# Performance work log

Measured on AMD Instinct MI355X. Metric: run time of the kernel, lower is better.

Reference implementation:

```python
import jax, jax.numpy as jnp
import numpy as np

DIM = 1024
HEADS = 16
HEAD_DIM = DIM // HEADS
SCALE = DIM ** (-0.5)  # note: module scales by full dim, not head_dim


def setup_inputs() -> dict:
    key = jax.random.key(0)
    k1, k2, k3, k4 = jax.random.split(key, 4)
    B, N = 4, 2048
    x = jax.random.normal(k1, (B, N, DIM), dtype=jnp.float32)
    # nn.Linear(dim, 3*dim, bias=False): weight [3*dim, dim]
    w_qkv = jax.random.normal(k2, (3 * DIM, DIM), dtype=jnp.float32) * (DIM ** -0.5)
    # nn.Linear(dim, dim) with bias
    w_out = jax.random.normal(k3, (DIM, DIM), dtype=jnp.float32) * (DIM ** -0.5)
    b_out = jax.random.normal(k4, (DIM,), dtype=jnp.float32) * 0.01
    return {"x": x, "w_qkv": w_qkv, "w_out": w_out, "b_out": b_out}


def reference(x, w_qkv, w_out, b_out):
    b, n, _ = x.shape
    qkv = jnp.einsum('bnd,ed->bne', x, w_qkv)  # [b, n, 3*dim]
    # rearrange 'b n (qkv h d) -> qkv b h n d'
    qkv = qkv.reshape(b, n, 3, HEADS, HEAD_DIM)
    q, k, v = (qkv[:, :, i].transpose(0, 2, 1, 3) for i in range(3))  # [b, h, n, d]
    dots = jnp.einsum('bhid,bhjd->bhij', q, k) * SCALE
    attn = jax.nn.softmax(dots, axis=-1)
    out = jnp.einsum('bhij,bhjd->bhid', attn, v)
    out = out.transpose(0, 2, 1, 3).reshape(b, n, HEADS * HEAD_DIM)  # [b, n, dim]
    return jnp.einsum('bnd,ed->bne', out, w_out) + b_out
```

## Files before the change

kernel.cpp:

```cpp
#include <hip/hip_runtime.h>

typedef __bf16 bf16_t;
typedef __bf16 bf16x2 __attribute__((ext_vector_type(2)));
typedef __bf16 bf16x4 __attribute__((ext_vector_type(4)));
typedef __bf16 bf16x8 __attribute__((ext_vector_type(8)));
typedef float floatx4 __attribute__((ext_vector_type(4)));

__device__ __forceinline__ void gll16(const void* g, void* l) {
  __builtin_amdgcn_global_load_lds(
      (const __attribute__((address_space(1))) void*)g,
      (__attribute__((address_space(3))) void*)l, 16, 0, 0);
}

__device__ __forceinline__ bf16x8 cvt8(const float4 a, const float4 b) {
  bf16x8 v;
  v[0] = (bf16_t)a.x; v[1] = (bf16_t)a.y; v[2] = (bf16_t)a.z; v[3] = (bf16_t)a.w;
  v[4] = (bf16_t)b.x; v[5] = (bf16_t)b.y; v[6] = (bf16_t)b.z; v[7] = (bf16_t)b.w;
  return v;
}

__global__ __launch_bounds__(256)
void cvt_f32_bf16(const float* __restrict__ src, bf16_t* __restrict__ dst, int n8)
{
  const int i = blockIdx.x * 256 + threadIdx.x;
  if (i < n8) {
    const float4 a = ((const float4*)src)[2 * i];
    const float4 b = ((const float4*)src)[2 * i + 1];
    *(bf16x8*)(dst + (size_t)i * 8) = cvt8(a, b);
  }
}

template<bool A32, bool W32, bool C32>
__global__ __launch_bounds__(256, 2)
void gemm_bt(const void* __restrict__ Av, const void* __restrict__ Wv,
             const float* __restrict__ bias, void* __restrict__ Cv,
             int M, int Nf, int K, int lda)
{
  __shared__ __align__(16) bf16_t lA[128 * 32];
  __shared__ __align__(16) bf16_t lB[128 * 32];

  const int tid  = threadIdx.x;
  const int wave = tid >> 6;
  const int lane = tid & 63;
  const int q    = lane >> 4;
  const int ln   = lane & 15;
  const int wm   = wave >> 1, wn = wave & 1;

  const int nwg = gridDim.x;
  const int bid = (blockIdx.x & 7) * (nwg >> 3) + (blockIdx.x >> 3);

  const int mtiles = M >> 7;
  const int mt = bid % mtiles;
  const int nt = bid / mtiles;
  const int m0 = mt << 7, n0 = nt << 7;

  floatx4 acc[4][4] = {};

  for (int k0 = 0; k0 < K; k0 += 32) {
    if constexpr (A32) {
      const float* Af = (const float*)Av;
#pragma unroll
      for (int sub = 0; sub < 2; ++sub) {
        const int r  = sub * 64 + (tid >> 2);
        const int c8 = tid & 3;
        const float* s = Af + (size_t)(m0 + r) * lda + k0 + c8 * 8;
        const float4 f0 = *(const float4*)s;
        const float4 f1 = *(const float4*)(s + 4);
        *(bf16x8*)(lA + r * 32 + (c8 ^ ((r >> 1) & 3)) * 8) = cvt8(f0, f1);
      }
    } else {
      const bf16_t* Ab = (const bf16_t*)Av;
#pragma unroll
      for (int half = 0; half < 2; ++half) {
        const int rbase = half * 64 + wave * 16;
        const int r  = rbase + (lane >> 2);
        const int gc = (lane & 3) ^ ((r >> 1) & 3);
        gll16(Ab + (size_t)(m0 + r) * lda + k0 + gc * 8, lA + rbase * 32);
      }
    }
    if constexpr (W32) {
      const float* Wf = (const float*)Wv;
#pragma unroll
      for (int sub = 0; sub < 2; ++sub) {
        const int r  = sub * 64 + (tid >> 2);
        const int c8 = tid & 3;
        const float* s = Wf + (size_t)(n0 + r) * K + k0 + c8 * 8;
        const float4 f0 = *(const float4*)s;
        const float4 f1 = *(const float4*)(s + 4);
        *(bf16x8*)(lB + r * 32 + (c8 ^ ((r >> 1) & 3)) * 8) = cvt8(f0, f1);
      }
    } else {
      const bf16_t* Wb = (const bf16_t*)Wv;
#pragma unroll
      for (int half = 0; half < 2; ++half) {
        const int rbase = half * 64 + wave * 16;
        const int r  = rbase + (lane >> 2);
        const int gc = (lane & 3) ^ ((r >> 1) & 3);
        gll16(Wb + (size_t)(n0 + r) * K + k0 + gc * 8, lB + rbase * 32);
      }
    }
    __syncthreads();

    bf16x8 af[4], bfr[4];
#pragma unroll
    for (int i = 0; i < 4; ++i) {
      const int r = wm * 64 + i * 16 + ln;
      af[i] = *(const bf16x8*)(lA + r * 32 + (q ^ ((r >> 1) & 3)) * 8);
    }
#pragma unroll
    for (int j = 0; j < 4; ++j) {
      const int r = wn * 64 + j * 16 + ln;
      bfr[j] = *(const bf16x8*)(lB + r * 32 + (q ^ ((r >> 1) & 3)) * 8);
    }
#pragma unroll
    for (int i = 0; i < 4; ++i)
#pragma unroll
      for (int j = 0; j < 4; ++j)
        acc[i][j] = __builtin_amdgcn_mfma_f32_16x16x32_bf16(af[i], bfr[j], acc[i][j], 0, 0, 0);
    __syncthreads();
  }

#pragma unroll
  for (int j = 0; j < 4; ++j) {
    const int col = n0 + wn * 64 + j * 16 + ln;
    const float bv = bias ? bias[col] : 0.0f;
#pragma unroll
    for (int i = 0; i < 4; ++i) {
      const int row = m0 + wm * 64 + i * 16 + q * 4;
#pragma unroll
      for (int r = 0; r < 4; ++r) {
        const float val = acc[i][j][r] + bv;
        if constexpr (C32)
          ((float*)Cv)[(size_t)(row + r) * Nf + col] = val;
        else
          ((bf16_t*)Cv)[(size_t)(row + r) * Nf + col] = (bf16_t)val;
      }
    }
  }
}

__global__ __launch_bounds__(256, 2)
void attn_kernel(bf16_t* __restrict__ qkv)
{
  __shared__ __align__(16) bf16_t lK[2][128 * 64];
  __shared__ __align__(16) bf16_t lVT[64 * 128];
  __shared__ __align__(16) bf16_t lP[128 * 128];

  const int tid  = threadIdx.x;
  const int wave = tid >> 6;
  const int lane = tid & 63;
  const int q  = lane >> 4;
  const int ln = lane & 15;
  const int wm = wave >> 1, wn = wave & 1;

  const int hw = blockIdx.x;
  const int w  = (hw & 7) * 128 + (hw >> 3);
  const int qt = w & 15;
  const int h  = (w >> 4) & 15;
  const int b  = w >> 8;

  bf16_t* Qbase = qkv + (size_t)(b * 2048 + qt * 128) * 3072 + h * 64;
  const bf16_t* Kbase = qkv + (size_t)(b * 2048) * 3072 + 1024 + h * 64;
  const bf16_t* Vbase = qkv + (size_t)(b * 2048) * 3072 + 2048 + h * 64;

#pragma unroll
  for (int t = 0; t < 4; ++t) {
    const int rbase = t * 32 + wave * 8;
    const int r  = rbase + (lane >> 3);
    const int gc = (lane & 7) ^ (r & 7);
    gll16(Qbase + (size_t)r * 3072 + gc * 8, lP + rbase * 64);
    gll16(Kbase + (size_t)r * 3072 + gc * 8, lK[0] + rbase * 64);
  }
  __syncthreads();

  bf16x8 qf[4][2];
#pragma unroll
  for (int i = 0; i < 4; ++i) {
    const int r = wm * 64 + i * 16 + ln;
#pragma unroll
    for (int kt = 0; kt < 2; ++kt) {
      const int c = (kt * 4 + q) ^ (r & 7);
      qf[i][kt] = *(const bf16x8*)(lP + r * 64 + c * 8);
    }
  }

  bf16x8 vcur[2][2], vnxt[2][2];
#pragma unroll
  for (int it = 0; it < 2; ++it) {
    const bf16_t* src = Vbase + (size_t)(2 * lane) * 3072 + (wave + it * 4) * 8;
    vcur[it][0] = *(const bf16x8*)src;
    vcur[it][1] = *(const bf16x8*)(src + 3072);
  }

  floatx4 accO[4][2] = {};
  floatx4 accS[4] = {};

  bf16x8 ones;
#pragma unroll
  for (int j = 0; j < 8; ++j) ones[j] = (bf16_t)1.0f;

  for (int jt = 0; jt < 16; ++jt) {
    const bf16_t* lKc = lK[jt & 1];
    bf16_t*       lKn = lK[(jt & 1) ^ 1];

    __syncthreads();

#pragma unroll
    for (int it = 0; it < 2; ++it) {
      const int c = wave + it * 4;
#pragma unroll
      for (int j = 0; j < 8; ++j) {
        const int d  = c * 8 + j;
        const int ch = (lane >> 2) ^ (d & 7);
        bf16x2 pr;
        pr[0] = vcur[it][0][j];
        pr[1] = vcur[it][1][j];
        *(bf16x2*)(lVT + d * 128 + ch * 8 + ((2 * lane) & 7)) = pr;
      }
    }

    bf16x8 kf[4][2];
#pragma unroll
    for (int n = 0; n < 4; ++n) {
      const int r = wn * 64 + n * 16 + ln;
#pragma unroll
      for (int kt = 0; kt < 2; ++kt) {
        const int c = (kt * 4 + q) ^ (r & 7);
        kf[n][kt] = *(const bf16x8*)(lKc + r * 64 + c * 8);
      }
    }

    if (jt < 15) {
      const int j0n = (jt + 1) * 128;
#pragma unroll
      for (int t = 0; t < 4; ++t) {
        const int rbase = t * 32 + wave * 8;
        const int r  = rbase + (lane >> 3);
        const int gc = (lane & 7) ^ (r & 7);
        gll16(Kbase + (size_t)(j0n + r) * 3072 + gc * 8, lKn + rbase * 64);
      }
#pragma unroll
      for (int it = 0; it < 2; ++it) {
        const bf16_t* src = Vbase + (size_t)(j0n + 2 * lane) * 3072 + (wave + it * 4) * 8;
        vnxt[it][0] = *(const bf16x8*)src;
        vnxt[it][1] = *(const bf16x8*)(src + 3072);
      }
    }

    __builtin_amdgcn_s_setprio(1);
#pragma unroll
    for (int i = 0; i < 4; ++i) {
#pragma unroll
      for (int n = 0; n < 4; ++n) {
        floatx4 st = {0.0f, 0.0f, 0.0f, 0.0f};
        st = __builtin_amdgcn_mfma_f32_16x16x32_bf16(kf[i][0], qf[n][0], st, 0, 0, 0);
        st = __builtin_amdgcn_mfma_f32_16x16x32_bf16(kf[i][1], qf[n][1], st, 0, 0, 0);
        bf16x4 pk;
#pragma unroll
        for (int r = 0; r < 4; ++r)
          pk[r] = (bf16_t)__builtin_amdgcn_exp2f(st[r] * 0.04508422f);
        const int m    = wm * 64 + n * 16 + ln;
        const int tok0 = wn * 64 + i * 16 + q * 4;
        *(bf16x4*)(lP + m * 128 + (((tok0 >> 3) ^ (m & 7)) << 3) + (tok0 & 7)) = pk;
      }
    }
    __builtin_amdgcn_s_setprio(0);

    __syncthreads();

    __builtin_amdgcn_s_setprio(1);
#pragma unroll
    for (int ks = 0; ks < 4; ++ks) {
      bf16x8 bv[2];
#pragma unroll
      for (int n = 0; n < 2; ++n) {
        const int d  = wn * 32 + n * 16 + ln;
        const int cc = (ks * 4 + q) ^ (d & 7);
        bv[n] = *(const bf16x8*)(lVT + d * 128 + cc * 8);
      }
#pragma unroll
      for (int i = 0; i < 4; ++i) {
        const int m = wm * 64 + i * 16 + ln;
        const bf16x8 ap = *(const bf16x8*)(lP + m * 128 + (((ks * 4 + q) ^ (m & 7)) << 3));
        accO[i][0] = __builtin_amdgcn_mfma_f32_16x16x32_bf16(ap, bv[0], accO[i][0], 0, 0, 0);
        accO[i][1] = __builtin_amdgcn_mfma_f32_16x16x32_bf16(ap, bv[1], accO[i][1], 0, 0, 0);
        accS[i]    = __builtin_amdgcn_mfma_f32_16x16x32_bf16(ap, ones,  accS[i],    0, 0, 0);
      }
    }
    __builtin_amdgcn_s_setprio(0);

    if (jt < 15) {
#pragma unroll
      for (int it = 0; it < 2; ++it) {
        vcur[it][0] = vnxt[it][0];
        vcur[it][1] = vnxt[it][1];
      }
    }
  }

#pragma unroll
  for (int i = 0; i < 4; ++i) {
#pragma unroll
    for (int r = 0; r < 4; ++r) {
      const int row = wm * 64 + i * 16 + q * 4 + r;
      const float rcp = 1.0f / fmaxf(accS[i][r], 1e-20f);
#pragma unroll
      for (int n = 0; n < 2; ++n) {
        const int col = wn * 32 + n * 16 + ln;
        Qbase[(size_t)row * 3072 + col] = (bf16_t)(accO[i][n][r] * rcp);
      }
    }
  }
}

extern "C" void kernel_launch(void* const* d_in, const int* in_sizes, int n_in,
                              void* d_out, int out_size, void* d_ws, size_t ws_size,
                              hipStream_t stream)
{
  const float* x     = (const float*)d_in[0];
  const float* w_qkv = (const float*)d_in[1];
  const float* w_out = (const float*)d_in[2];
  const float* b_out = (const float*)d_in[3];
  float* out = (float*)d_out;

  bf16_t* qkv    = (bf16_t*)d_ws;
  bf16_t* xb     = qkv    + (size_t)8192 * 3072;
  bf16_t* wqkvb  = xb     + (size_t)8192 * 1024;
  bf16_t* woutb  = wqkvb  + (size_t)3072 * 1024;

  cvt_f32_bf16<<<dim3(4096), dim3(256), 0, stream>>>(x,     xb,    8192 * 1024 / 8);
  cvt_f32_bf16<<<dim3(1536), dim3(256), 0, stream>>>(w_qkv, wqkvb, 3072 * 1024 / 8);
  cvt_f32_bf16<<<dim3(512),  dim3(256), 0, stream>>>(w_out, woutb, 1024 * 1024 / 8);

  gemm_bt<false, false, false><<<dim3(64 * 24), dim3(256), 0, stream>>>(
      xb, wqkvb, nullptr, qkv, 8192, 3072, 1024, 1024);
  attn_kernel<<<dim3(1024), dim3(256), 0, stream>>>(qkv);
  gemm_bt<false, false, true><<<dim3(64 * 8), dim3(256), 0, stream>>>(
      qkv, woutb, b_out, out, 8192, 1024, 1024, 3072);
}
```

Baseline: 292.4 us.

## Fold softmax scale into QKV GEMM epilogue, rework PV wave split and tile mapping

Moves the softmax scale multiply (including the log2e factor) from the attention exp2 loop into the QKV GEMM epilogue, applied to the Q columns only. This removes one multiply per score element in the inner loop. The PV stage now gives each wave 32 rows by the full 64-wide head dim instead of a 64x32 quadrant, which cuts redundant row-sum MFMAs and duplicated P fragment reads. GEMM block-to-tile mapping changes to a fixed 8x8 grouping that assumes 64 M-tiles.

```diff
diff --git a/kernel.cpp b/kernel.cpp
--- a/kernel.cpp
+++ b/kernel.cpp
@@ -34,7 +34,7 @@
 __global__ __launch_bounds__(256, 2)
 void gemm_bt(const void* __restrict__ Av, const void* __restrict__ Wv,
              const float* __restrict__ bias, void* __restrict__ Cv,
-             int M, int Nf, int K, int lda)
+             int M, int Nf, int K, int lda, int qcols, float qscale)
 {
   __shared__ __align__(16) bf16_t lA[128 * 32];
   __shared__ __align__(16) bf16_t lB[128 * 32];
@@ -46,12 +46,10 @@
   const int ln   = lane & 15;
   const int wm   = wave >> 1, wn = wave & 1;
 
-  const int nwg = gridDim.x;
-  const int bid = (blockIdx.x & 7) * (nwg >> 3) + (blockIdx.x >> 3);
-
-  const int mtiles = M >> 7;
-  const int mt = bid % mtiles;
-  const int nt = bid / mtiles;
+  const int x     = blockIdx.x & 7;
+  const int local = blockIdx.x >> 3;
+  const int mt = x * 8 + (local & 7);
+  const int nt = local >> 3;
   const int m0 = mt << 7, n0 = nt << 7;
 
   floatx4 acc[4][4] = {};
@@ -124,12 +122,13 @@
   for (int j = 0; j < 4; ++j) {
     const int col = n0 + wn * 64 + j * 16 + ln;
     const float bv = bias ? bias[col] : 0.0f;
+    const float sc = (col < qcols) ? qscale : 1.0f;
 #pragma unroll
     for (int i = 0; i < 4; ++i) {
       const int row = m0 + wm * 64 + i * 16 + q * 4;
 #pragma unroll
       for (int r = 0; r < 4; ++r) {
-        const float val = acc[i][j][r] + bv;
+        const float val = acc[i][j][r] * sc + bv;
         if constexpr (C32)
           ((float*)Cv)[(size_t)(row + r) * Nf + col] = val;
         else
@@ -192,8 +191,8 @@
     vcur[it][1] = *(const bf16x8*)(src + 3072);
   }
 
-  floatx4 accO[4][2] = {};
-  floatx4 accS[4] = {};
+  floatx4 accO[2][4] = {};
+  floatx4 accS[2] = {};
 
   bf16x8 ones;
 #pragma unroll
@@ -258,7 +257,7 @@
         bf16x4 pk;
 #pragma unroll
         for (int r = 0; r < 4; ++r)
-          pk[r] = (bf16_t)__builtin_amdgcn_exp2f(st[r] * 0.04508422f);
+          pk[r] = (bf16_t)__builtin_amdgcn_exp2f(st[r]);
         const int m    = wm * 64 + n * 16 + ln;
         const int tok0 = wn * 64 + i * 16 + q * 4;
         *(bf16x4*)(lP + m * 128 + (((tok0 >> 3) ^ (m & 7)) << 3) + (tok0 & 7)) = pk;
@@ -271,20 +270,21 @@
     __builtin_amdgcn_s_setprio(1);
 #pragma unroll
     for (int ks = 0; ks < 4; ++ks) {
-      bf16x8 bv[2];
-#pragma unroll
-      for (int n = 0; n < 2; ++n) {
-        const int d  = wn * 32 + n * 16 + ln;
+      bf16x8 bv[4];
+#pragma unroll
+      for (int n = 0; n < 4; ++n) {
+        const int d  = n * 16 + ln;
         const int cc = (ks * 4 + q) ^ (d & 7);
         bv[n] = *(const bf16x8*)(lVT + d * 128 + cc * 8);
       }
 #pragma unroll
-      for (int i = 0; i < 4; ++i) {
-        const int m = wm * 64 + i * 16 + ln;
+      for (int i = 0; i < 2; ++i) {
+        const int m = wave * 32 + i * 16 + ln;
         const bf16x8 ap = *(const bf16x8*)(lP + m * 128 + (((ks * 4 + q) ^ (m & 7)) << 3));
-        accO[i][0] = __builtin_amdgcn_mfma_f32_16x16x32_bf16(ap, bv[0], accO[i][0], 0, 0, 0);
-        accO[i][1] = __builtin_amdgcn_mfma_f32_16x16x32_bf16(ap, bv[1], accO[i][1], 0, 0, 0);
-        accS[i]    = __builtin_amdgcn_mfma_f32_16x16x32_bf16(ap, ones,  accS[i],    0, 0, 0);
+#pragma unroll
+        for (int n = 0; n < 4; ++n)
+          accO[i][n] = __builtin_amdgcn_mfma_f32_16x16x32_bf16(ap, bv[n], accO[i][n], 0, 0, 0);
+        accS[i] = __builtin_amdgcn_mfma_f32_16x16x32_bf16(ap, ones, accS[i], 0, 0, 0);
       }
     }
     __builtin_amdgcn_s_setprio(0);
@@ -299,14 +299,14 @@
   }
 
 #pragma unroll
-  for (int i = 0; i < 4; ++i) {
+  for (int i = 0; i < 2; ++i) {
 #pragma unroll
     for (int r = 0; r < 4; ++r) {
-      const int row = wm * 64 + i * 16 + q * 4 + r;
+      const int row = wave * 32 + i * 16 + q * 4 + r;
       const float rcp = 1.0f / fmaxf(accS[i][r], 1e-20f);
 #pragma unroll
-      for (int n = 0; n < 2; ++n) {
-        const int col = wn * 32 + n * 16 + ln;
+      for (int n = 0; n < 4; ++n) {
+        const int col = n * 16 + ln;
         Qbase[(size_t)row * 3072 + col] = (bf16_t)(accO[i][n][r] * rcp);
       }
     }
@@ -328,13 +328,15 @@
   bf16_t* wqkvb  = xb     + (size_t)8192 * 1024;
   bf16_t* woutb  = wqkvb  + (size_t)3072 * 1024;
 
+  const float qs = 0.04508422f;
+
   cvt_f32_bf16<<<dim3(4096), dim3(256), 0, stream>>>(x,     xb,    8192 * 1024 / 8);
   cvt_f32_bf16<<<dim3(1536), dim3(256), 0, stream>>>(w_qkv, wqkvb, 3072 * 1024 / 8);
   cvt_f32_bf16<<<dim3(512),  dim3(256), 0, stream>>>(w_out, woutb, 1024 * 1024 / 8);
 
   gemm_bt<false, false, false><<<dim3(64 * 24), dim3(256), 0, stream>>>(
-      xb, wqkvb, nullptr, qkv, 8192, 3072, 1024, 1024);
+      xb, wqkvb, nullptr, qkv, 8192, 3072, 1024, 1024, 1024, qs);
   attn_kernel<<<dim3(1024), dim3(256), 0, stream>>>(qkv);
   gemm_bt<false, false, true><<<dim3(64 * 8), dim3(256), 0, stream>>>(
-      qkv, woutb, b_out, out, 8192, 1024, 1024, 3072);
-}
+      qkv, woutb, b_out, out, 8192, 1024, 1024, 3072, 0, 1.0f);
+}
```

Result: faster. 276.2 us (-5.6%).
